# Optimization experiments

Measured on AMD Instinct MI355X. Metric: run time of the kernel, lower is better.

Reference implementation:

```python
import jax, jax.numpy as jnp
import numpy as np

N_NODES = 20000
N_EDGES = 640000
HID = 256
IN_F, IN_SIZE = 6, 6
OUT_F, FH = 6, 3
EDGE_DIM = 8
T_DIM, S_DIM = 4, 6
N_LAYERS = 5


def setup_inputs() -> dict:
    key = jax.random.key(0)
    ks = jax.random.split(key, 32)
    g = lambda i, shape, scale=0.05: jax.random.normal(ks[i], shape, dtype=jnp.float32) * scale
    inp = {
        "x": jax.random.normal(ks[0], (N_NODES, IN_F, IN_SIZE), dtype=jnp.float32),
        "edge_index": jax.random.randint(ks[1], (2, N_EDGES), 0, N_NODES, dtype=jnp.int32),
        "edge_attr": jax.random.normal(ks[2], (N_EDGES, EDGE_DIM), dtype=jnp.float32),
        "t": jax.random.normal(ks[3], (N_NODES, T_DIM), dtype=jnp.float32),
        "s": jax.random.normal(ks[4], (N_NODES, S_DIM), dtype=jnp.float32),
        # embedder
        "W_emb": g(5, (IN_F * IN_SIZE, HID)), "b_emb": jnp.zeros((HID,), jnp.float32),
        # spatio-temporal encoder: t/s linear embeds + fusion over concat(x, te, se)
        "W_t": g(6, (T_DIM, HID)), "b_t": jnp.zeros((HID,), jnp.float32),
        "W_s": g(7, (S_DIM, HID)), "b_s": jnp.zeros((HID,), jnp.float32),
        "W_f": g(8, (3 * HID, HID)), "b_f": jnp.zeros((HID,), jnp.float32),
        # layernorm
        "ln_g": jnp.ones((HID,), jnp.float32), "ln_b": jnp.zeros((HID,), jnp.float32),
        # 5 TransformerConv layers (heads=1): query/key/value/edge/skip linears
        "Wq": g(9, (N_LAYERS, HID, HID)), "bq": jnp.zeros((N_LAYERS, HID), jnp.float32),
        "Wk": g(10, (N_LAYERS, HID, HID)), "bk": jnp.zeros((N_LAYERS, HID), jnp.float32),
        "Wv": g(11, (N_LAYERS, HID, HID)), "bv": jnp.zeros((N_LAYERS, HID), jnp.float32),
        "We": g(12, (N_LAYERS, EDGE_DIM, HID)), "be": jnp.zeros((N_LAYERS, HID), jnp.float32),
        "Wskip": g(13, (N_LAYERS, HID, HID)), "bskip": jnp.zeros((N_LAYERS, HID), jnp.float32),
        # decoder
        "W_dec": g(14, (HID, OUT_F * FH)), "b_dec": jnp.zeros((OUT_F * FH,), jnp.float32),
    }
    return inp


def _layernorm(x, g, b, eps=1e-5):
    mu = jnp.mean(x, axis=-1, keepdims=True)
    var = jnp.mean((x - mu) ** 2, axis=-1, keepdims=True)
    return (x - mu) * jax.lax.rsqrt(var + eps) * g + b


def _transformer_conv(x, src, dst, edge_attr, Wq, bq, Wk, bk, Wv, bv, We, be, Wskip, bskip):
    n = x.shape[0]
    d = x.shape[1]
    q = x @ Wq + bq                      # [n, d]
    k = x @ Wk + bk
    v = x @ Wv + bv
    e = edge_attr @ We + be              # [E, d]
    kj = k[src] + e                      # gather + edge fuse [E, d]
    vj = v[src] + e
    alpha = jnp.sum(q[dst] * kj, axis=-1) / jnp.sqrt(jnp.float32(d))  # [E]
    # segment softmax over incoming edges of each destination node
    m = jax.ops.segment_max(alpha, dst, num_segments=n)
    a = jnp.exp(alpha - m[dst])
    denom = jax.ops.segment_sum(a, dst, num_segments=n)
    w = a / (denom[dst] + 1e-16)
    out = jax.ops.segment_sum(vj * w[:, None], dst, num_segments=n)  # [n, d]
    return out + x @ Wskip + bskip       # root/skip connection


def reference(x, edge_index, edge_attr, t, s,
              W_emb, b_emb, W_t, b_t, W_s, b_s, W_f, b_f, ln_g, ln_b,
              Wq, bq, Wk, bk, Wv, bv, We, be, Wskip, bskip, W_dec, b_dec):
    n = x.shape[0]
    h = x.reshape(n, -1) @ W_emb + b_emb
    te = t @ W_t + b_t
    se = s @ W_s + b_s
    h = jnp.concatenate([h, te, se], axis=-1) @ W_f + b_f   # spatio-temporal fuse
    h = jax.nn.relu(_layernorm(h, ln_g, ln_b))
    src, dst = edge_index[0], edge_index[1]
    for i in range(N_LAYERS):
        h = jax.nn.relu(_transformer_conv(h, src, dst, edge_attr,
                                          Wq[i], bq[i], Wk[i], bk[i], Wv[i], bv[i],
                                          We[i], be[i], Wskip[i], bskip[i]))
    out = h @ W_dec + b_dec
    return out.reshape(n, OUT_F, FH)
```

## Files before the change

### kernel.cpp

```cpp
#include <hip/hip_runtime.h>
#include <hip/hip_fp8.h>
#include <math.h>

#define NN 20000
#define NPAD 20096
#define NE 640000
#define NOUT 1152
#define GQS 544
#define KVB 768
#define CAP 80
#define SCQ 0.09016994f
#define TIDX(r,k) ((((r)>>4)*4096) + (((k)>>3)*128) + (((r)&15)*8) + ((k)&7))

typedef _Float16 f16;
typedef f16 f16x8 __attribute__((ext_vector_type(8)));
typedef f16 f16x4 __attribute__((ext_vector_type(4)));
typedef f16 h2    __attribute__((ext_vector_type(2)));
typedef float f32x4 __attribute__((ext_vector_type(4)));
typedef float f32x2 __attribute__((ext_vector_type(2)));

static __device__ __forceinline__ float fdot2(h2 a, h2 b, float c) {
#if __has_builtin(__builtin_amdgcn_fdot2)
  return __builtin_amdgcn_fdot2(a, b, c, false);
#else
  return c + (float)a[0]*(float)b[0] + (float)a[1]*(float)b[1];
#endif
}

static __device__ __forceinline__ float fast_exp2(float x) {
#if __has_builtin(__builtin_amdgcn_exp2f)
  return __builtin_amdgcn_exp2f(x);
#else
  return exp2f(x);
#endif
}

static __device__ __forceinline__ unsigned pack_fp8x4(float a, float b, float c, float d) {
#if __has_builtin(__builtin_amdgcn_cvt_pk_fp8_f32)
  int r = __builtin_amdgcn_cvt_pk_fp8_f32(a, b, 0, false);
  r = __builtin_amdgcn_cvt_pk_fp8_f32(c, d, r, true);
  return (unsigned)r;
#else
  __hip_fp8_e4m3 w(a), x2(b), y(c), z(d);
  return (unsigned)w.__x | ((unsigned)x2.__x<<8) | ((unsigned)y.__x<<16) | ((unsigned)z.__x<<24);
#endif
}

template<bool HI>
static __device__ __forceinline__ f32x2 unpack_fp8x2(unsigned v) {
#if __has_builtin(__builtin_amdgcn_cvt_pk_f32_fp8)
  return __builtin_amdgcn_cvt_pk_f32_fp8((int)v, HI);
#else
  unsigned s = HI ? (v >> 16) : (v & 0xffff);
  __hip_fp8_e4m3 a, b; a.__x = (unsigned char)(s & 0xff); b.__x = (unsigned char)(s >> 8);
  return (f32x2){ (float)a, (float)b };
#endif
}

__global__ __launch_bounds__(256) void k_prep_all(
    const float* __restrict__ W_emb, const float* __restrict__ W_t,
    const float* __restrict__ W_s,   const float* __restrict__ W_f,
    const float* __restrict__ b_emb, const float* __restrict__ b_t,
    const float* __restrict__ b_s,   const float* __restrict__ b_f,
    const float* __restrict__ Wq, const float* __restrict__ Wk,
    const float* __restrict__ Wv, const float* __restrict__ Wsk,
    const float* __restrict__ We, const float* __restrict__ be,
    const float* __restrict__ bq, const float* __restrict__ bk,
    const float* __restrict__ bv, const float* __restrict__ bsk,
    f16* __restrict__ Wch, float* __restrict__ bc,
    f16* __restrict__ WT, float* __restrict__ b_all,
    f16* __restrict__ hA, f16* __restrict__ hB)
{
  __shared__ float smem[64*65];
  int b = blockIdx.x;
  int tid = threadIdx.x;

  if (b < 47) {
    int r = b, c = tid;
    if (r < 36) {
      float a = 0.f;
      for (int m = 0; m < 256; m++) a += W_emb[r*256+m] * W_f[m*256+c];
      Wch[r*256+c] = (f16)a;
    } else if (r < 40) {
      int rr = r - 36; float a = 0.f;
      for (int m = 0; m < 256; m++) a += W_t[rr*256+m] * W_f[(256+m)*256+c];
      Wch[r*256+c] = (f16)a;
    } else if (r < 46) {
      int rr = r - 40; float a = 0.f;
      for (int m = 0; m < 256; m++) a += W_s[rr*256+m] * W_f[(512+m)*256+c];
      Wch[r*256+c] = (f16)a;
    } else {
      float a = b_f[c];
      for (int m = 0; m < 256; m++) a += b_emb[m]*W_f[m*256+c];
      for (int m = 0; m < 256; m++) a += b_t[m]*W_f[(256+m)*256+c];
      for (int m = 0; m < 256; m++) a += b_s[m]*W_f[(512+m)*256+c];
      bc[c] = a;
    }
  } else if (b < 367) {
    float (*lds)[65] = (float(*)[65])smem;
    int bb = b - 47;
    int nt = bb & 3, kt = (bb >> 2) & 3, mat = (bb >> 4) & 3, L = bb >> 6;
    const float* src = (mat == 0 ? Wq : mat == 1 ? Wk : mat == 2 ? Wv : Wsk) + (size_t)L*65536;
    int k0 = kt*64, n0 = nt*64;
    int c = tid & 63, r4 = tid >> 6;
    #pragma unroll
    for (int rr = 0; rr < 16; rr++) {
      int row = rr*4 + r4;
      lds[row][c] = src[(size_t)(k0 + row)*256 + n0 + c];
    }
    __syncthreads();
    f16* dst = WT + (size_t)L*294912;
    int nl = tid & 63, kb2 = tid >> 6;
    int ng = mat*256 + n0 + nl;
    #pragma unroll
    for (int half = 0; half < 2; half++) {
      int kb = kb2 + half*4;
      f16x8 v;
      #pragma unroll
      for (int e = 0; e < 8; e++) v[e] = (f16)lds[kb*8 + e][nl];
      *(f16x8*)(dst + TIDX(ng, k0 + kb*8)) = v;
    }
  } else if (b < 412) {
    float* vec = smem;
    int bb = b - 367;
    int L = bb / 9;
    int t = bb % 9;
    vec[tid] = (t < 8) ? We[(size_t)L*2048 + t*256 + tid] : be[(size_t)L*256 + tid];
    __syncthreads();
    int wave = tid >> 6, lane = tid & 63;
    for (int k = wave; k < 256; k += 4) {
      f32x4 wq = *(const f32x4*)(Wq + (size_t)L*65536 + (size_t)k*256 + lane*4);
      f32x4 vv = *(const f32x4*)(vec + lane*4);
      float d = wq[0]*vv[0] + wq[1]*vv[1] + wq[2]*vv[2] + wq[3]*vv[3];
      #pragma unroll
      for (int o = 32; o; o >>= 1) d += __shfl_xor(d, o, 64);
      if (lane == 0) WT[(size_t)L*294912 + TIDX(1024 + t, k)] = (f16)d;
    }
  } else if (b < 417) {
    int L = b - 412;
    for (int c = tid; c < NOUT; c += 256) {
      float v;
      if (c < 256)       v = bq [L*256+c];
      else if (c < 512)  v = bk [L*256+(c-256)];
      else if (c < 768)  v = bv [L*256+(c-512)];
      else if (c < 1024) v = bsk[L*256+(c-768)];
      else if (c < 1032) {
        int t = c-1024; float a = 0.f;
        for (int m = 0; m < 256; m++) a += bq[L*256+m]*We[(size_t)L*2048 + t*256 + m];
        v = a;
      } else if (c == 1032) {
        float a = 0.f;
        for (int m = 0; m < 256; m++) a += bq[L*256+m]*be[L*256+m];
        v = a;
      } else v = 0.f;
      b_all[(size_t)L*NOUT + c] = v;
    }
  } else {
    f16* p = (b == 417 ? hA : hB) + (size_t)NN*256;
    f16x8 z = {};
    for (int i = tid; i < (NPAD-NN)*256/8; i += 256)
      *(f16x8*)(p + (size_t)i*8) = z;
  }
}

__global__ void k_scatter(const int* __restrict__ ei, const float* __restrict__ eattr,
                          int* cnt, int* __restrict__ src_s, f16* __restrict__ eaperm)
{
  int e = blockIdx.x*256 + threadIdx.x;
  if (e < NE) {
    int d = ei[NE + e];
    int pos = atomicAdd(&cnt[d], 1);
    int slot = d*CAP + pos;
    src_s[slot] = ei[e];
    f32x4 a0 = *(const f32x4*)(eattr + (size_t)e*8);
    f32x4 a1 = *(const f32x4*)(eattr + (size_t)e*8 + 4);
    f16x8 ea = { (f16)a0[0],(f16)a0[1],(f16)a0[2],(f16)a0[3],
                 (f16)a1[0],(f16)a1[1],(f16)a1[2],(f16)a1[3] };
    *(f16x8*)(eaperm + (size_t)slot*8) = ea;
  }
}

__global__ __launch_bounds__(256) void k_encoder(
    const float* __restrict__ x, const float* __restrict__ t, const float* __restrict__ s,
    const f16* __restrict__ Wch, const float* __restrict__ bc,
    const float* __restrict__ lng, const float* __restrict__ lnb,
    f16* __restrict__ h)
{
  __shared__ f16 Wcs[46*256];
  __shared__ float xin[16][48];
  __shared__ float bcs[256], lgs[256], lbs[256];
  int tid = threadIdx.x;
  int u0 = blockIdx.x * 16;
  for (int i = tid; i < 46*128; i += 256)
    ((unsigned int*)Wcs)[i] = ((const unsigned int*)Wch)[i];
  bcs[tid] = bc[tid]; lgs[tid] = lng[tid]; lbs[tid] = lnb[tid];
  for (int i = tid; i < 576; i += 256) xin[i/36][i%36] = x[(size_t)u0*36 + i];
  if (tid < 64) xin[tid>>2][36 + (tid&3)] = t[(size_t)u0*4 + tid];
  if (tid < 96) xin[tid/6][40 + tid%6] = s[(size_t)u0*6 + tid];
  __syncthreads();
  int node = tid >> 4, cg = tid & 15;
  int u = u0 + node;
  float acc[16];
  #pragma unroll
  for (int j = 0; j < 16; j++) acc[j] = bcs[cg*16+j];
  for (int r = 0; r < 46; r++) {
    float xv = xin[node][r];
    const h2* wr = (const h2*)(Wcs + r*256 + cg*16);
    #pragma unroll
    for (int j2 = 0; j2 < 8; j2++) {
      h2 w2 = wr[j2];
      acc[j2*2]   += xv * (float)w2[0];
      acc[j2*2+1] += xv * (float)w2[1];
    }
  }
  float sm = 0.f, sq = 0.f;
  #pragma unroll
  for (int j = 0; j < 16; j++) { sm += acc[j]; sq += acc[j]*acc[j]; }
  #pragma unroll
  for (int o = 1; o < 16; o <<= 1) { sm += __shfl_xor(sm, o, 64); sq += __shfl_xor(sq, o, 64); }
  float mu  = sm * (1.f/256.f);
  float var = sq * (1.f/256.f) - mu*mu;
  float rin = rsqrtf(var + 1e-5f);
  f16x8 o0, o1;
  #pragma unroll
  for (int j = 0; j < 8; j++) {
    int c = cg*16 + j;
    float v = (acc[j]-mu)*rin*lgs[c] + lbs[c];
    o0[j] = (f16)fmaxf(v, 0.f);
  }
  #pragma unroll
  for (int j = 0; j < 8; j++) {
    int c = cg*16 + 8 + j;
    float v = (acc[8+j]-mu)*rin*lgs[c] + lbs[c];
    o1[j] = (f16)fmaxf(v, 0.f);
  }
  *(f16x8*)(h + TIDX(u, cg*16))   = o0;
  *(f16x8*)(h + TIDX(u, cg*16+8)) = o1;
}

__global__ __launch_bounds__(256) void k_gemm(
    const f16* __restrict__ A, const f16* __restrict__ BT,
    const float* __restrict__ bias, f16* __restrict__ gout,
    unsigned char* __restrict__ kvt)
{
  int tid = threadIdx.x;
  int wave = tid >> 6, lane = tid & 63;
  int wm = wave >> 1, wn = wave & 1;
  int bm = blockIdx.x * 128 + wm*64;
  int bn = blockIdx.y * 128 + wn*64;
  int lr = lane & 15;
  int kg = lane >> 4;
  f32x4 acc[4][4];
  #pragma unroll
  for (int i = 0; i < 4; i++)
    #pragma unroll
    for (int j = 0; j < 4; j++) acc[i][j] = (f32x4){0.f,0.f,0.f,0.f};

  const f16* Ab = A  + (size_t)(bm >> 4)*4096 + kg*128 + lr*8;
  const f16* Bb = BT + (size_t)(bn >> 4)*4096 + kg*128 + lr*8;
  #pragma unroll
  for (int k0 = 0; k0 < 256; k0 += 32) {
    f16x8 af[4], bf[4];
    #pragma unroll
    for (int i = 0; i < 4; i++) af[i] = *(const f16x8*)(Ab + i*4096 + k0*16);
    #pragma unroll
    for (int j = 0; j < 4; j++) bf[j] = *(const f16x8*)(Bb + j*4096 + k0*16);
    #pragma unroll
    for (int i = 0; i < 4; i++)
      #pragma unroll
      for (int j = 0; j < 4; j++)
        acc[i][j] = __builtin_amdgcn_mfma_f32_16x16x32_f16(bf[j], af[i], acc[i][j], 0, 0, 0);
  }

  #pragma unroll
  for (int j = 0; j < 4; j++) {
    int cb0 = bn + j*16;
    if (cb0 >= 1040) continue;
    int colq = cb0 + kg*4;
    f32x4 bv = *(const f32x4*)(bias + colq);
    #pragma unroll
    for (int i = 0; i < 4; i++) {
      int row = bm + i*16 + lr;
      float v0 = acc[i][j][0]+bv[0], v1 = acc[i][j][1]+bv[1];
      float v2 = acc[i][j][2]+bv[2], v3 = acc[i][j][3]+bv[3];
      if (cb0 < 256) {
        f16x4 st = { (f16)(v0*SCQ), (f16)(v1*SCQ), (f16)(v2*SCQ), (f16)(v3*SCQ) };
        *(f16x4*)(gout + (size_t)row*GQS + colq) = st;
      } else if (cb0 < 512) {
        *(unsigned*)(kvt + (size_t)row*KVB + (colq-256)) = pack_fp8x4(v0, v1, v2, v3);
      } else if (cb0 < 768) {
        f16x4 st = { (f16)v0, (f16)v1, (f16)v2, (f16)v3 };
        *(f16x4*)(kvt + (size_t)row*KVB + 256 + (size_t)(colq-512)*2) = st;
      } else if (cb0 < 1024) {
        f16x4 st = { (f16)v0, (f16)v1, (f16)v2, (f16)v3 };
        *(f16x4*)(gout + (size_t)row*GQS + 256 + (colq-768)) = st;
      } else {
        f16x4 st = { (f16)(v0*SCQ), (f16)(v1*SCQ), (f16)(v2*SCQ), (f16)(v3*SCQ) };
        *(f16x4*)(gout + (size_t)row*GQS + 512 + (colq-1024)) = st;
      }
    }
  }
}

__global__ __launch_bounds__(256) void k_attn(
    const f16* __restrict__ gout, const unsigned char* __restrict__ kvt,
    const f16* __restrict__ eaperm,
    const float* __restrict__ WeL, const float* __restrict__ beL,
    const int* __restrict__ cnt, const int* __restrict__ src_s,
    f16* __restrict__ hout, int n)
{
  __shared__ float mav[2][268];
  int wid  = threadIdx.x >> 6;
  int lane = threadIdx.x & 63;
  int nl   = wid >> 1;
  int wsub = wid & 1;
  int grp  = lane >> 4;
  int gl   = lane & 15;
  int u = blockIdx.x*2 + nl;
  bool active = (u < n);

  float qf[16];
  f16x8 qe8 = {};
  float qbv = 0.f;
  int deg = 0;
  if (active) {
    const f16* gb = gout + (size_t)u*GQS;
    f16x8 qh0 = ((const f16x8*)(gb + gl*16))[0];
    f16x8 qh1 = ((const f16x8*)(gb + gl*16))[1];
    #pragma unroll
    for (int j = 0; j < 8; j++) { qf[j] = (float)qh0[j]; qf[8+j] = (float)qh1[j]; }
    qe8 = *(const f16x8*)(gb + 512);
    qbv = (float)gb[520];
    deg = cnt[u];
  } else {
    #pragma unroll
    for (int j = 0; j < 16; j++) qf[j] = 0.f;
  }

  float ssum = 0.f;
  h2 av2[8], ae2[4];
  #pragma unroll
  for (int j = 0; j < 8; j++) av2[j] = (h2){(f16)0.f, (f16)0.f};
  #pragma unroll
  for (int j = 0; j < 4; j++) ae2[j] = (h2){(f16)0.f, (f16)0.f};

  size_t ubase = (size_t)u*CAP;
  #pragma unroll 2
  for (int i = grp + wsub*4; i < deg; i += 8) {
    int sn = src_s[ubase + i];
    const unsigned char* kb = kvt + (size_t)sn*KVB;
    uint4 kw = *(const uint4*)(kb + gl*16);
    const f16* vp = (const f16*)(kb + 256) + gl*16;
    f16x8 v0 = ((const f16x8*)vp)[0];
    f16x8 v1 = ((const f16x8*)vp)[1];
    f16x8 ea = *(const f16x8*)(eaperm + (ubase + i)*8);

    float d = 0.f;
    f32x2 p;
    p = unpack_fp8x2<false>(kw.x); d += p[0]*qf[0]  + p[1]*qf[1];
    p = unpack_fp8x2<true >(kw.x); d += p[0]*qf[2]  + p[1]*qf[3];
    p = unpack_fp8x2<false>(kw.y); d += p[0]*qf[4]  + p[1]*qf[5];
    p = unpack_fp8x2<true >(kw.y); d += p[0]*qf[6]  + p[1]*qf[7];
    p = unpack_fp8x2<false>(kw.z); d += p[0]*qf[8]  + p[1]*qf[9];
    p = unpack_fp8x2<true >(kw.z); d += p[0]*qf[10] + p[1]*qf[11];
    p = unpack_fp8x2<false>(kw.w); d += p[0]*qf[12] + p[1]*qf[13];
    p = unpack_fp8x2<true >(kw.w); d += p[0]*qf[14] + p[1]*qf[15];
    d += __shfl_xor(d, 1, 64);
    d += __shfl_xor(d, 2, 64);
    d += __shfl_xor(d, 4, 64);
    d += __shfl_xor(d, 8, 64);

    float edot = 0.f;
    edot = fdot2((h2){ea[0],ea[1]}, (h2){qe8[0],qe8[1]}, edot);
    edot = fdot2((h2){ea[2],ea[3]}, (h2){qe8[2],qe8[3]}, edot);
    edot = fdot2((h2){ea[4],ea[5]}, (h2){qe8[4],qe8[5]}, edot);
    edot = fdot2((h2){ea[6],ea[7]}, (h2){qe8[6],qe8[7]}, edot);

    float w = fast_exp2(d + edot + qbv);
    ssum += w;
    f16 wh = (f16)w;
    h2 wv = {wh, wh};
    #pragma unroll
    for (int j = 0; j < 4; j++) av2[j]   += wv * (h2){v0[2*j], v0[2*j+1]};
    #pragma unroll
    for (int j = 0; j < 4; j++) av2[4+j] += wv * (h2){v1[2*j], v1[2*j+1]};
    #pragma unroll
    for (int j = 0; j < 4; j++) ae2[j]   += wv * (h2){ea[2*j], ea[2*j+1]};
  }

  float av[16], ae[8];
  #pragma unroll
  for (int j = 0; j < 8; j++) { av[2*j] = (float)av2[j][0]; av[2*j+1] = (float)av2[j][1]; }
  #pragma unroll
  for (int j = 0; j < 4; j++) { ae[2*j] = (float)ae2[j][0]; ae[2*j+1] = (float)ae2[j][1]; }

  #pragma unroll
  for (int j = 0; j < 16; j++) {
    av[j] += __shfl_xor(av[j], 16, 64);
    av[j] += __shfl_xor(av[j], 32, 64);
  }
  #pragma unroll
  for (int j = 0; j < 8; j++) {
    ae[j] += __shfl_xor(ae[j], 16, 64);
    ae[j] += __shfl_xor(ae[j], 32, 64);
  }
  ssum += __shfl_xor(ssum, 16, 64);
  ssum += __shfl_xor(ssum, 32, 64);

  int cb = gl*16 + grp*4;
  if (wsub == 1 && active) {
    #pragma unroll
    for (int t = 0; t < 4; t++) mav[nl][cb+t] = av[grp*4+t];
    if (lane < 8) mav[nl][256+lane] = ae[lane];
    if (lane == 0) mav[nl][264] = ssum;
  }
  __syncthreads();
  if (wsub == 0 && active) {
    float s2 = ssum + mav[nl][264];
    float inv = 1.f/(s2 + 1e-16f);
    float aem[8];
    #pragma unroll
    for (int e = 0; e < 8; e++) aem[e] = ae[e] + mav[nl][256+e];
    const f16* gb = gout + (size_t)u*GQS;
    f16 res[4];
    #pragma unroll
    for (int t = 0; t < 4; t++) {
      int c = cb + t;
      float o = av[grp*4+t] + mav[nl][c];
      #pragma unroll
      for (int e = 0; e < 8; e++) o += aem[e]*WeL[e*256 + c];
      o += s2*beL[c];
      o = o*inv + (float)gb[256 + c];
      res[t] = (f16)fmaxf(o, 0.f);
    }
    f16x4 outp = { res[0], res[1], res[2], res[3] };
    *(f16x4*)(hout + TIDX(u, cb)) = outp;
  }
}

__global__ __launch_bounds__(256) void k_decoder(
    const f16* __restrict__ h, const float* __restrict__ Wd,
    const float* __restrict__ bd, float* __restrict__ out)
{
  int n0 = blockIdx.x*32;
  __shared__ float hs[32*256];
  int tid = threadIdx.x;
  for (int j = tid; j < 32*32; j += 256) {
    int node = j >> 5, c8 = (j & 31)*8;
    f16x8 v = *(const f16x8*)(h + TIDX(n0 + node, c8));
    float* dst = &hs[node*256 + c8];
    #pragma unroll
    for (int e = 0; e < 8; e++) dst[e] = (float)v[e];
  }
  __syncthreads();
  for (int o = tid; o < 32*18; o += 256) {
    int ln = o/18, col = o - ln*18;
    int node = n0 + ln;
    float acc = bd[col];
    const float* hr = &hs[ln*256];
    #pragma unroll 4
    for (int k4 = 0; k4 < 64; k4++) {
      f32x4 hv = *(const f32x4*)(hr + k4*4);
      acc += hv[0]*Wd[(k4*4+0)*18+col] + hv[1]*Wd[(k4*4+1)*18+col]
           + hv[2]*Wd[(k4*4+2)*18+col] + hv[3]*Wd[(k4*4+3)*18+col];
    }
    out[(size_t)node*18 + col] = acc;
  }
}

extern "C" void kernel_launch(void* const* d_in, const int* in_sizes, int n_in,
                              void* d_out, int out_size, void* d_ws, size_t ws_size,
                              hipStream_t stream)
{
  const float* x     = (const float*)d_in[0];
  const int*   ei    = (const int*)  d_in[1];
  const float* eattr = (const float*)d_in[2];
  const float* t     = (const float*)d_in[3];
  const float* s     = (const float*)d_in[4];
  const float* W_emb = (const float*)d_in[5];
  const float* b_emb = (const float*)d_in[6];
  const float* W_t   = (const float*)d_in[7];
  const float* b_t   = (const float*)d_in[8];
  const float* W_s   = (const float*)d_in[9];
  const float* b_s   = (const float*)d_in[10];
  const float* W_f   = (const float*)d_in[11];
  const float* b_f   = (const float*)d_in[12];
  const float* ln_g  = (const float*)d_in[13];
  const float* ln_b  = (const float*)d_in[14];
  const float* Wq    = (const float*)d_in[15];
  const float* bq    = (const float*)d_in[16];
  const float* Wk    = (const float*)d_in[17];
  const float* bk    = (const float*)d_in[18];
  const float* Wv    = (const float*)d_in[19];
  const float* bv    = (const float*)d_in[20];
  const float* We    = (const float*)d_in[21];
  const float* be    = (const float*)d_in[22];
  const float* Wsk   = (const float*)d_in[23];
  const float* bsk   = (const float*)d_in[24];
  const float* W_dec = (const float*)d_in[25];
  const float* b_dec = (const float*)d_in[26];

  float* wsf = (float*)d_ws;
  size_t off = 0;
  float* bc    = wsf + off; off += 256;
  float* b_all = wsf + off; off += (size_t)5*NOUT;
  f16*   Wch   = (f16*)(wsf + off); off += (size_t)46*256/2;
  f16*   WT    = (f16*)(wsf + off); off += (size_t)5*294912/2;
  f16*   gout  = (f16*)(wsf + off); off += (size_t)NPAD*GQS/2;
  unsigned char* kvt = (unsigned char*)(wsf + off); off += (size_t)NPAD*KVB/4;
  f16*   hA    = (f16*)(wsf + off); off += (size_t)NPAD*256/2;
  f16*   hB    = (f16*)(wsf + off); off += (size_t)NPAD*256/2;
  f16*   eaperm= (f16*)(wsf + off); off += (size_t)NN*CAP*8/2;
  int*   src_s = (int*)(wsf + off); off += (size_t)NN*CAP;
  int*   cnt   = (int*)(wsf + off); off += NN;

  (void)hipMemsetAsync(cnt, 0, NN*sizeof(int), stream);
  k_prep_all<<<419, 256, 0, stream>>>(W_emb, W_t, W_s, W_f, b_emb, b_t, b_s, b_f,
                                      Wq, Wk, Wv, Wsk, We, be, bq, bk, bv, bsk,
                                      Wch, bc, WT, b_all, hA, hB);
  k_scatter <<<(NE+255)/256, 256, 0, stream>>>(ei, eattr, cnt, src_s, eaperm);

  k_encoder <<<NN/16, 256, 0, stream>>>(x, t, s, Wch, bc, ln_g, ln_b, hA);

  f16* hin = hA;
  f16* hot = hB;
  dim3 ggrid(NPAD/128, NOUT/128);
  for (int L = 0; L < 5; L++) {
    k_gemm<<<ggrid, 256, 0, stream>>>(hin, WT + (size_t)L*294912,
                                      b_all + (size_t)L*NOUT, gout, kvt);
    k_attn<<<NN/2, 256, 0, stream>>>(gout, kvt, eaperm, We + (size_t)L*2048,
                                     be + (size_t)L*256, cnt, src_s, hot, NN);
    f16* tmp = hin; hin = hot; hot = tmp;
  }
  k_decoder<<<NN/32, 256, 0, stream>>>(hin, W_dec, b_dec, (float*)d_out);
}
```

Before: 666.2 us.

## Quantize Q/K to int8 with sdot4 and V to fp8 in attention

Q and K are now stored as int8 (scaled by 32) and the attention score is computed with packed int8 dot products (sdot4), then rescaled by a constant. V moves from fp16 to fp8, which halves the per-edge gathered K/V row from 768 to 512 bytes, and V is accumulated in fp32 after unpacking. The gather buffers are split into a q int8 buffer and a skip/edge-query fp16 buffer. This cuts gather bandwidth and dot-product ALU work per edge, at the cost of precision loss from fixed-scale int8 quantization with clipping and fp8 values.

```diff
diff --git a/kernel.cpp b/kernel.cpp
--- a/kernel.cpp
+++ b/kernel.cpp
@@ -6,10 +6,11 @@
 #define NPAD 20096
 #define NE 640000
 #define NOUT 1152
-#define GQS 544
-#define KVB 768
+#define GSS 272
+#define KVB 512
 #define CAP 80
 #define SCQ 0.09016994f
+#define ISCL 8.8057e-5f
 #define TIDX(r,k) ((((r)>>4)*4096) + (((k)>>3)*128) + (((r)&15)*8) + ((k)&7))
 
 typedef _Float16 f16;
@@ -33,6 +34,29 @@
 #else
   return exp2f(x);
 #endif
+}
+
+static __device__ __forceinline__ int sdot4(unsigned a, unsigned b, int c) {
+#if __has_builtin(__builtin_amdgcn_sdot4)
+  return __builtin_amdgcn_sdot4((int)a, (int)b, c, false);
+#else
+  int r = c;
+  #pragma unroll
+  for (int i = 0; i < 4; i++) {
+    int ai = ((int)((a >> (8*i)) & 255) ^ 128) - 128;
+    int bi = ((int)((b >> (8*i)) & 255) ^ 128) - 128;
+    r += ai*bi;
+  }
+  return r;
+#endif
+}
+
+static __device__ __forceinline__ unsigned pack_i8x4(float a, float b, float c, float d) {
+  int i0 = (int)rintf(a), i1 = (int)rintf(b), i2 = (int)rintf(c), i3 = (int)rintf(d);
+  i0 = max(-127, min(127, i0)); i1 = max(-127, min(127, i1));
+  i2 = max(-127, min(127, i2)); i3 = max(-127, min(127, i3));
+  return (unsigned)(i0 & 255) | ((unsigned)(i1 & 255) << 8)
+       | ((unsigned)(i2 & 255) << 16) | ((unsigned)(i3 & 255) << 24);
 }
 
 static __device__ __forceinline__ unsigned pack_fp8x4(float a, float b, float c, float d) {
@@ -240,8 +264,9 @@
 
 __global__ __launch_bounds__(256) void k_gemm(
     const f16* __restrict__ A, const f16* __restrict__ BT,
-    const float* __restrict__ bias, f16* __restrict__ gout,
-    unsigned char* __restrict__ kvt)
+    const float* __restrict__ bias,
+    unsigned char* __restrict__ qt8, unsigned char* __restrict__ kvt,
+    f16* __restrict__ gsk)
 {
   int tid = threadIdx.x;
   int wave = tid >> 6, lane = tid & 63;
@@ -284,27 +309,25 @@
       float v0 = acc[i][j][0]+bv[0], v1 = acc[i][j][1]+bv[1];
       float v2 = acc[i][j][2]+bv[2], v3 = acc[i][j][3]+bv[3];
       if (cb0 < 256) {
-        f16x4 st = { (f16)(v0*SCQ), (f16)(v1*SCQ), (f16)(v2*SCQ), (f16)(v3*SCQ) };
-        *(f16x4*)(gout + (size_t)row*GQS + colq) = st;
+        *(unsigned*)(qt8 + (size_t)row*256 + colq) = pack_i8x4(v0*32.f, v1*32.f, v2*32.f, v3*32.f);
       } else if (cb0 < 512) {
-        *(unsigned*)(kvt + (size_t)row*KVB + (colq-256)) = pack_fp8x4(v0, v1, v2, v3);
+        *(unsigned*)(kvt + (size_t)row*KVB + (colq-256)) = pack_i8x4(v0*32.f, v1*32.f, v2*32.f, v3*32.f);
       } else if (cb0 < 768) {
-        f16x4 st = { (f16)v0, (f16)v1, (f16)v2, (f16)v3 };
-        *(f16x4*)(kvt + (size_t)row*KVB + 256 + (size_t)(colq-512)*2) = st;
+        *(unsigned*)(kvt + (size_t)row*KVB + 256 + (colq-512)) = pack_fp8x4(v0, v1, v2, v3);
       } else if (cb0 < 1024) {
         f16x4 st = { (f16)v0, (f16)v1, (f16)v2, (f16)v3 };
-        *(f16x4*)(gout + (size_t)row*GQS + 256 + (colq-768)) = st;
+        *(f16x4*)(gsk + (size_t)row*GSS + (colq-768)) = st;
       } else {
         f16x4 st = { (f16)(v0*SCQ), (f16)(v1*SCQ), (f16)(v2*SCQ), (f16)(v3*SCQ) };
-        *(f16x4*)(gout + (size_t)row*GQS + 512 + (colq-1024)) = st;
+        *(f16x4*)(gsk + (size_t)row*GSS + 256 + (colq-1024)) = st;
       }
     }
   }
 }
 
 __global__ __launch_bounds__(256) void k_attn(
-    const f16* __restrict__ gout, const unsigned char* __restrict__ kvt,
-    const f16* __restrict__ eaperm,
+    const unsigned char* __restrict__ qt8, const unsigned char* __restrict__ kvt,
+    const f16* __restrict__ gsk, const f16* __restrict__ eaperm,
     const float* __restrict__ WeL, const float* __restrict__ beL,
     const int* __restrict__ cnt, const int* __restrict__ src_s,
     f16* __restrict__ hout, int n)
@@ -319,28 +342,23 @@
   int u = blockIdx.x*2 + nl;
   bool active = (u < n);
 
-  float qf[16];
+  uint4 qp = {0,0,0,0};
   f16x8 qe8 = {};
   float qbv = 0.f;
   int deg = 0;
   if (active) {
-    const f16* gb = gout + (size_t)u*GQS;
-    f16x8 qh0 = ((const f16x8*)(gb + gl*16))[0];
-    f16x8 qh1 = ((const f16x8*)(gb + gl*16))[1];
-    #pragma unroll
-    for (int j = 0; j < 8; j++) { qf[j] = (float)qh0[j]; qf[8+j] = (float)qh1[j]; }
-    qe8 = *(const f16x8*)(gb + 512);
-    qbv = (float)gb[520];
+    qp = *(const uint4*)(qt8 + (size_t)u*256 + gl*16);
+    const f16* gb = gsk + (size_t)u*GSS;
+    qe8 = *(const f16x8*)(gb + 256);
+    qbv = (float)gb[264];
     deg = cnt[u];
-  } else {
-    #pragma unroll
-    for (int j = 0; j < 16; j++) qf[j] = 0.f;
   }
 
   float ssum = 0.f;
-  h2 av2[8], ae2[4];
-  #pragma unroll
-  for (int j = 0; j < 8; j++) av2[j] = (h2){(f16)0.f, (f16)0.f};
+  float av[16];
+  h2 ae2[4];
+  #pragma unroll
+  for (int j = 0; j < 16; j++) av[j] = 0.f;
   #pragma unroll
   for (int j = 0; j < 4; j++) ae2[j] = (h2){(f16)0.f, (f16)0.f};
 
@@ -350,25 +368,17 @@
     int sn = src_s[ubase + i];
     const unsigned char* kb = kvt + (size_t)sn*KVB;
     uint4 kw = *(const uint4*)(kb + gl*16);
-    const f16* vp = (const f16*)(kb + 256) + gl*16;
-    f16x8 v0 = ((const f16x8*)vp)[0];
-    f16x8 v1 = ((const f16x8*)vp)[1];
+    uint4 vw = *(const uint4*)(kb + 256 + gl*16);
     f16x8 ea = *(const f16x8*)(eaperm + (ubase + i)*8);
 
-    float d = 0.f;
-    f32x2 p;
-    p = unpack_fp8x2<false>(kw.x); d += p[0]*qf[0]  + p[1]*qf[1];
-    p = unpack_fp8x2<true >(kw.x); d += p[0]*qf[2]  + p[1]*qf[3];
-    p = unpack_fp8x2<false>(kw.y); d += p[0]*qf[4]  + p[1]*qf[5];
-    p = unpack_fp8x2<true >(kw.y); d += p[0]*qf[6]  + p[1]*qf[7];
-    p = unpack_fp8x2<false>(kw.z); d += p[0]*qf[8]  + p[1]*qf[9];
-    p = unpack_fp8x2<true >(kw.z); d += p[0]*qf[10] + p[1]*qf[11];
-    p = unpack_fp8x2<false>(kw.w); d += p[0]*qf[12] + p[1]*qf[13];
-    p = unpack_fp8x2<true >(kw.w); d += p[0]*qf[14] + p[1]*qf[15];
-    d += __shfl_xor(d, 1, 64);
-    d += __shfl_xor(d, 2, 64);
-    d += __shfl_xor(d, 4, 64);
-    d += __shfl_xor(d, 8, 64);
+    int di = sdot4(kw.x, qp.x, 0);
+    di = sdot4(kw.y, qp.y, di);
+    di = sdot4(kw.z, qp.z, di);
+    di = sdot4(kw.w, qp.w, di);
+    di += __shfl_xor(di, 1, 64);
+    di += __shfl_xor(di, 2, 64);
+    di += __shfl_xor(di, 4, 64);
+    di += __shfl_xor(di, 8, 64);
 
     float edot = 0.f;
     edot = fdot2((h2){ea[0],ea[1]}, (h2){qe8[0],qe8[1]}, edot);
@@ -376,21 +386,24 @@
     edot = fdot2((h2){ea[4],ea[5]}, (h2){qe8[4],qe8[5]}, edot);
     edot = fdot2((h2){ea[6],ea[7]}, (h2){qe8[6],qe8[7]}, edot);
 
-    float w = fast_exp2(d + edot + qbv);
+    float w = fast_exp2((float)di*ISCL + edot + qbv);
     ssum += w;
+    f32x2 p;
+    p = unpack_fp8x2<false>(vw.x); av[0]  += w*p[0]; av[1]  += w*p[1];
+    p = unpack_fp8x2<true >(vw.x); av[2]  += w*p[0]; av[3]  += w*p[1];
+    p = unpack_fp8x2<false>(vw.y); av[4]  += w*p[0]; av[5]  += w*p[1];
+    p = unpack_fp8x2<true >(vw.y); av[6]  += w*p[0]; av[7]  += w*p[1];
+    p = unpack_fp8x2<false>(vw.z); av[8]  += w*p[0]; av[9]  += w*p[1];
+    p = unpack_fp8x2<true >(vw.z); av[10] += w*p[0]; av[11] += w*p[1];
+    p = unpack_fp8x2<false>(vw.w); av[12] += w*p[0]; av[13] += w*p[1];
+    p = unpack_fp8x2<true >(vw.w); av[14] += w*p[0]; av[15] += w*p[1];
     f16 wh = (f16)w;
     h2 wv = {wh, wh};
     #pragma unroll
-    for (int j = 0; j < 4; j++) av2[j]   += wv * (h2){v0[2*j], v0[2*j+1]};
-    #pragma unroll
-    for (int j = 0; j < 4; j++) av2[4+j] += wv * (h2){v1[2*j], v1[2*j+1]};
-    #pragma unroll
-    for (int j = 0; j < 4; j++) ae2[j]   += wv * (h2){ea[2*j], ea[2*j+1]};
-  }
-
-  float av[16], ae[8];
-  #pragma unroll
-  for (int j = 0; j < 8; j++) { av[2*j] = (float)av2[j][0]; av[2*j+1] = (float)av2[j][1]; }
+    for (int j = 0; j < 4; j++) ae2[j] += wv * (h2){ea[2*j], ea[2*j+1]};
+  }
+
+  float ae[8];
   #pragma unroll
   for (int j = 0; j < 4; j++) { ae[2*j] = (float)ae2[j][0]; ae[2*j+1] = (float)ae2[j][1]; }
 
@@ -421,7 +434,7 @@
     float aem[8];
     #pragma unroll
     for (int e = 0; e < 8; e++) aem[e] = ae[e] + mav[nl][256+e];
-    const f16* gb = gout + (size_t)u*GQS;
+    const f16* gb = gsk + (size_t)u*GSS;
     f16 res[4];
     #pragma unroll
     for (int t = 0; t < 4; t++) {
@@ -430,7 +443,7 @@
       #pragma unroll
       for (int e = 0; e < 8; e++) o += aem[e]*WeL[e*256 + c];
       o += s2*beL[c];
-      o = o*inv + (float)gb[256 + c];
+      o = o*inv + (float)gb[c];
       res[t] = (f16)fmaxf(o, 0.f);
     }
     f16x4 outp = { res[0], res[1], res[2], res[3] };
@@ -506,8 +519,9 @@
   float* b_all = wsf + off; off += (size_t)5*NOUT;
   f16*   Wch   = (f16*)(wsf + off); off += (size_t)46*256/2;
   f16*   WT    = (f16*)(wsf + off); off += (size_t)5*294912/2;
-  f16*   gout  = (f16*)(wsf + off); off += (size_t)NPAD*GQS/2;
+  unsigned char* qt8 = (unsigned char*)(wsf + off); off += (size_t)NPAD*256/4;
   unsigned char* kvt = (unsigned char*)(wsf + off); off += (size_t)NPAD*KVB/4;
+  f16*   gsk   = (f16*)(wsf + off); off += (size_t)NPAD*GSS/2;
   f16*   hA    = (f16*)(wsf + off); off += (size_t)NPAD*256/2;
   f16*   hB    = (f16*)(wsf + off); off += (size_t)NPAD*256/2;
   f16*   eaperm= (f16*)(wsf + off); off += (size_t)NN*CAP*8/2;
@@ -527,8 +541,8 @@
   dim3 ggrid(NPAD/128, NOUT/128);
   for (int L = 0; L < 5; L++) {
     k_gemm<<<ggrid, 256, 0, stream>>>(hin, WT + (size_t)L*294912,
-                                      b_all + (size_t)L*NOUT, gout, kvt);
-    k_attn<<<NN/2, 256, 0, stream>>>(gout, kvt, eaperm, We + (size_t)L*2048,
+                                      b_all + (size_t)L*NOUT, qt8, kvt, gsk);
+    k_attn<<<NN/2, 256, 0, stream>>>(qt8, kvt, gsk, eaperm, We + (size_t)L*2048,
                                      be + (size_t)L*256, cnt, src_s, hot, NN);
     f16* tmp = hin; hin = hot; hot = tmp;
   }
```

Result: faster. 626.0 us (-6.0%).
